# Optimization experiments

Measured on AMD Instinct MI355X. Metric: run time of the kernel, lower is better.

Reference implementation:

```python
import jax, jax.numpy as jnp
import numpy as np
import math

B, L, H, NH = 8, 512, 512, 8
DH = H // NH


def setup_inputs() -> dict:
    key = jax.random.key(0)
    ks = jax.random.split(key, 12)
    src = jax.random.normal(ks[0], (B, L, H), dtype=jnp.float32)
    seq_len = jax.random.randint(ks[1], (B,), L // 2, L + 1).astype(jnp.int32)
    seq_len = seq_len.at[0].set(L)  # guarantee max(seq_len) == L
    pe = jax.random.normal(ks[2], (2 * L, H), dtype=jnp.float32) * 0.02
    s = 1.0 / math.sqrt(H)
    Wq = jax.random.normal(ks[3], (H, H), dtype=jnp.float32) * s
    bq = jnp.zeros((H,), jnp.float32)
    Wk = jax.random.normal(ks[4], (H, H), dtype=jnp.float32) * s
    bk = jnp.zeros((H,), jnp.float32)
    Wv = jax.random.normal(ks[5], (H, H), dtype=jnp.float32) * s
    bv = jnp.zeros((H,), jnp.float32)
    Wr = jax.random.normal(ks[6], (H, H), dtype=jnp.float32) * s
    br = jnp.zeros((H,), jnp.float32)
    u = jax.random.normal(ks[7], (NH, DH), dtype=jnp.float32) * 0.02
    v = jax.random.normal(ks[8], (NH, DH), dtype=jnp.float32) * 0.02
    gamma = jnp.ones((H,), jnp.float32)
    beta = jnp.zeros((H,), jnp.float32)
    return dict(src=src, seq_len=seq_len, pe=pe, Wq=Wq, bq=bq, Wk=Wk, bk=bk,
                Wv=Wv, bv=bv, Wr=Wr, br=br, u=u, v=v, gamma=gamma, beta=beta)


def reference(src, seq_len, pe, Wq, bq, Wk, bk, Wv, bv, Wr, br, u, v, gamma, beta):
    b, l, h = src.shape
    dh = h // NH
    # relative distance rel[i,j] = j - i, lookup pe[rel + L]  -> [L, L, H]
    rel = jnp.arange(l)[None, :] - jnp.arange(l)[:, None]
    R = pe[rel + l]
    # projections (torch Linear: y = x W^T + b)
    q = src @ Wq.T + bq
    k = src @ Wk.T + bk
    val = src @ Wv.T + bv
    R = R @ Wr.T + br
    # split heads
    q = q.reshape(b, l, NH, dh)
    k = k.reshape(b, l, NH, dh)
    val = val.reshape(b, l, NH, dh)
    R = R.reshape(l, l, NH, dh)
    # Transformer-XL score terms
    A = jnp.einsum('bihd,bjhd->bhij', q, k)
    Bt = jnp.einsum('bihd,ijhd->bhij', q, R)
    C = jnp.einsum('hd,bjhd->bhj', u, k)[:, :, None, :]
    D = jnp.einsum('ijhd,hd->hij', R, v)[None]
    scores = (A + Bt + C + D) / math.sqrt(dh)
    # key-side padding mask
    mask = jnp.arange(l)[None, :] < seq_len[:, None]  # [B, L]
    scores = jnp.where(mask[:, None, None, :], scores, jnp.float32(-1e15))
    attn = jax.nn.softmax(scores, axis=-1)
    out = jnp.einsum('bhij,bjhd->bihd', attn, val).reshape(b, l, h)
    res = src + out
    # LayerNorm (eps=1e-5) then exact GELU
    mu = jnp.mean(res, axis=-1, keepdims=True)
    var = jnp.mean((res - mu) ** 2, axis=-1, keepdims=True)
    ln = (res - mu) * jax.lax.rsqrt(var + 1e-5) * gamma + beta
    return jax.nn.gelu(ln, approximate=False)
```

## Files before the change

### kernel.cpp

```cpp
#include <hip/hip_runtime.h>
#include <math.h>

#define Bn 8
#define Ln 512
#define Hn 512
#define NHn 8
#define DHn 64

typedef __attribute__((ext_vector_type(8))) short short8;
typedef __attribute__((ext_vector_type(4))) float f32x4;

__device__ __forceinline__ unsigned short f2bf(float f) {
    unsigned int u = __float_as_uint(f);
    unsigned int r = (u + 0x7FFFu + ((u >> 16) & 1u)) >> 16;
    return (unsigned short)r;
}
__device__ __forceinline__ float bf2f(unsigned short s) {
    return __uint_as_float(((unsigned int)s) << 16);
}

__device__ __forceinline__ void gload_lds16(const void* g, void* l) {
    __builtin_amdgcn_global_load_lds(
        (const __attribute__((address_space(1))) unsigned int*)g,
        (__attribute__((address_space(3))) unsigned int*)l,
        16, 0, 0);
}

__global__ __launch_bounds__(256) void convert_kernel(
    const float* __restrict__ src, const float* __restrict__ pe,
    const float* __restrict__ Wq, const float* __restrict__ Wk,
    const float* __restrict__ Wv, const float* __restrict__ Wr,
    const float* __restrict__ bq, const float* __restrict__ bk,
    const float* __restrict__ bv,
    unsigned short* __restrict__ src_bf, unsigned short* __restrict__ pe_bf,
    unsigned short* __restrict__ Wcat_bf, unsigned short* __restrict__ Wr_bf,
    float* __restrict__ bcat)
{
    const int bid = blockIdx.x;
    const int tid = threadIdx.x;
    const float* in; unsigned short* outp; int base4;
    if (bid < 2048)      { in = src; outp = src_bf;           base4 = bid; }
    else if (bid < 2560) { in = pe;  outp = pe_bf;            base4 = bid - 2048; }
    else if (bid < 2816) { in = Wq;  outp = Wcat_bf;          base4 = bid - 2560; }
    else if (bid < 3072) { in = Wk;  outp = Wcat_bf + 262144; base4 = bid - 2816; }
    else if (bid < 3328) { in = Wv;  outp = Wcat_bf + 524288; base4 = bid - 3072; }
    else if (bid < 3584) { in = Wr;  outp = Wr_bf;            base4 = bid - 3328; }
    else {
        const int idx = (bid - 3584) * 256 + tid;
        if (idx < 512)            bcat[idx] = bq[idx];
        else if (idx < 1024)      bcat[idx] = bk[idx - 512];
        else if (idx < 1536)      bcat[idx] = bv[idx - 1024];
        return;
    }
    const int i4 = (base4 * 256 + tid) * 4;
    float4 x = *(const float4*)&in[i4];
    ushort4 o;
    o.x = f2bf(x.x); o.y = f2bf(x.y); o.z = f2bf(x.z); o.w = f2bf(x.w);
    *(ushort4*)&outp[i4] = o;
}

__global__ __launch_bounds__(256) void mfma_nt_kernel(
    const unsigned short* __restrict__ A0, const unsigned short* __restrict__ B0,
    const float* __restrict__ bias0, unsigned short* __restrict__ C0, int ldc0,
    const unsigned short* __restrict__ A1, const unsigned short* __restrict__ B1,
    const float* __restrict__ bias1, unsigned short* __restrict__ C1, int ldc1)
{
    const unsigned short* A; const unsigned short* B; const float* bias;
    unsigned short* C; int ldc;
    if (blockIdx.z == 0) {
        A = A0; B = B0; bias = bias0; C = C0; ldc = ldc0;
    } else {
        if (blockIdx.x >= 4 || blockIdx.y >= 8) return;
        A = A1; B = B1; bias = bias1; C = C1; ldc = ldc1;
    }

    __shared__ unsigned short As[128 * 32];
    __shared__ unsigned short Bs[128 * 32];

    const int m0 = blockIdx.y * 128;
    const int n0 = blockIdx.x * 128;
    const int t = threadIdx.x;
    const int wave = t >> 6, lane = t & 63;
    const int wm = (wave >> 1) * 64;
    const int wn = (wave & 1) * 64;

    f32x4 acc[4][4] = {};

    const int srow = wave * 32 + (lane >> 2);
    const int scol = (lane & 3) * 8;
    const unsigned short* Ag = A + (size_t)(m0 + srow) * 512 + scol;
    const unsigned short* Bg = B + (size_t)(n0 + srow) * 512 + scol;
    unsigned short* AsW = &As[srow * 32 + scol];
    unsigned short* BsW = &Bs[srow * 32 + scol];

    for (int k0 = 0; k0 < 512; k0 += 32) {
        __syncthreads();
        gload_lds16(Ag + k0,            AsW);
        gload_lds16(Ag + k0 + 16 * 512, AsW + 16 * 32);
        gload_lds16(Bg + k0,            BsW);
        gload_lds16(Bg + k0 + 16 * 512, BsW + 16 * 32);
        __syncthreads();

        short8 af[4], bf[4];
        #pragma unroll
        for (int mt = 0; mt < 4; ++mt)
            af[mt] = *(const short8*)&As[(wm + mt * 16 + (lane & 15)) * 32 + (lane >> 4) * 8];
        #pragma unroll
        for (int nt = 0; nt < 4; ++nt)
            bf[nt] = *(const short8*)&Bs[(wn + nt * 16 + (lane & 15)) * 32 + (lane >> 4) * 8];
        #pragma unroll
        for (int mt = 0; mt < 4; ++mt)
            #pragma unroll
            for (int nt = 0; nt < 4; ++nt)
                acc[mt][nt] = __builtin_amdgcn_mfma_f32_16x16x32_bf16(
                    af[mt], bf[nt], acc[mt][nt], 0, 0, 0);
    }

    const int crow = (lane >> 4) * 4;
    const int ccol = lane & 15;
    #pragma unroll
    for (int mt = 0; mt < 4; ++mt)
        #pragma unroll
        for (int nt = 0; nt < 4; ++nt) {
            const int n = n0 + wn + nt * 16 + ccol;
            const float bn = bias[n];
            #pragma unroll
            for (int r = 0; r < 4; ++r) {
                const int m = m0 + wm + mt * 16 + crow + r;
                C[(size_t)m * ldc + n] = f2bf(acc[mt][nt][r] + bn);
            }
        }
}

#define PADK 72
__global__ __launch_bounds__(256) void attn_kernel(
    const unsigned short* __restrict__ QKVb,
    const unsigned short* __restrict__ Rpb,
    const float* __restrict__ u, const float* __restrict__ v,
    const int* __restrict__ seq_len, float* __restrict__ O)
{
    const int i0 = blockIdx.x * 64;
    const int h  = blockIdx.y;
    const int b  = blockIdx.z;
    const int slen = seq_len[b];

    __shared__ unsigned short k_s [64 * PADK];
    __shared__ unsigned short vT_s[64 * PADK];
    __shared__ unsigned short rs_s[128 * PADK];
    __shared__ unsigned short p_s [4 * 16 * PADK];
    __shared__ unsigned short qrT [4 * 128 * 20];

    const int t = threadIdx.x;
    const int wave = t >> 6, lane = t & 63;
    const int l = lane & 15, g = lane >> 4;

    short8 af_qu[2], af_qv[2];
    {
        const unsigned short* qrow =
            QKVb + (size_t)(b * 512 + i0 + wave * 16 + l) * 1536 + h * 64;
        #pragma unroll
        for (int kk = 0; kk < 2; ++kk) {
            const int c = kk * 32 + g * 8;
            unsigned short q8[8];
            *(uint4*)q8 = *(const uint4*)(qrow + c);
            float4 u0 = *(const float4*)(u + h * 64 + c);
            float4 u1 = *(const float4*)(u + h * 64 + c + 4);
            float4 v0 = *(const float4*)(v + h * 64 + c);
            float4 v1 = *(const float4*)(v + h * 64 + c + 4);
            float uf[8] = {u0.x,u0.y,u0.z,u0.w,u1.x,u1.y,u1.z,u1.w};
            float vf[8] = {v0.x,v0.y,v0.z,v0.w,v1.x,v1.y,v1.z,v1.w};
            short8 qu, qv;
            #pragma unroll
            for (int e = 0; e < 8; ++e) {
                float qf = bf2f(q8[e]);
                qu[e] = (short)f2bf(qf + uf[e]);
                qv[e] = (short)f2bf(qf + vf[e]);
            }
            af_qu[kk] = qu; af_qv[kk] = qv;
        }
    }

    float m_run[4], l_run[4];
    f32x4 accO[4] = {};
    #pragma unroll
    for (int r = 0; r < 4; ++r) { m_run[r] = -3.0e38f; l_run[r] = 0.f; }

    const int dmin = i0 ? (0 - i0 + 449) : 449;

    for (int j0 = 0; j0 < 512; j0 += 64) {
        __syncthreads();

        {
            const int jr = t >> 2, c0 = (t & 3) * 16;
            const unsigned short* base =
                QKVb + (size_t)(b * 512 + j0 + jr) * 1536 + h * 64;
            uint4 kv0 = *(const uint4*)(base + 512 + c0);
            uint4 kv1 = *(const uint4*)(base + 512 + c0 + 8);
            *(uint4*)(k_s + jr * PADK + c0)     = kv0;
            *(uint4*)(k_s + jr * PADK + c0 + 8) = kv1;
            unsigned short vt[16];
            *(uint4*)vt       = *(const uint4*)(base + 1024 + c0);
            *(uint4*)(vt + 8) = *(const uint4*)(base + 1024 + c0 + 8);
            #pragma unroll
            for (int m = 0; m < 16; ++m)
                vT_s[(c0 + m) * PADK + jr] = vt[m];
        }
        {
            const int r = t >> 1, c0 = (t & 1) * 32;
            int grow = j0 - i0 + 449 + r;
            if (grow > 1023) grow = 1023;
            const unsigned short* rp = Rpb + (size_t)grow * 512 + h * 64 + c0;
            #pragma unroll
            for (int e = 0; e < 4; ++e)
                *(uint4*)(rs_s + r * PADK + c0 + e * 8) = *(const uint4*)(rp + e * 8);
        }
        __syncthreads();

        f32x4 accA[4];
        #pragma unroll
        for (int nt = 0; nt < 4; ++nt) {
            f32x4 a = {};
            #pragma unroll
            for (int kk = 0; kk < 2; ++kk) {
                short8 bk = *(const short8*)&k_s[(nt * 16 + l) * PADK + kk * 32 + g * 8];
                a = __builtin_amdgcn_mfma_f32_16x16x32_bf16(af_qu[kk], bk, a, 0, 0, 0);
            }
            accA[nt] = a;
        }

        #pragma unroll
        for (int nt8 = 0; nt8 < 8; ++nt8) {
            f32x4 a = {};
            #pragma unroll
            for (int kk = 0; kk < 2; ++kk) {
                short8 br8 = *(const short8*)&rs_s[(nt8 * 16 + l) * PADK + kk * 32 + g * 8];
                a = __builtin_amdgcn_mfma_f32_16x16x32_bf16(af_qv[kk], br8, a, 0, 0, 0);
            }
            ushort4 w4;
            w4.x = f2bf(a[0]); w4.y = f2bf(a[1]); w4.z = f2bf(a[2]); w4.w = f2bf(a[3]);
            *(ushort4*)(qrT + ((size_t)wave * 128 + nt8 * 16 + l) * 20 + g * 4) = w4;
        }
        __builtin_amdgcn_sched_barrier(0);

        float sv[4][4];
        #pragma unroll
        for (int nt = 0; nt < 4; ++nt)
            #pragma unroll
            for (int r = 0; r < 4; ++r) {
                const int i16 = g * 4 + r;
                const int band = nt * 16 + l - (wave * 16 + i16) + 63;
                const float qr = bf2f(qrT[((size_t)wave * 128 + band) * 20 + i16]);
                float s = (accA[nt][r] + qr) * 0.125f;
                if (j0 + nt * 16 + l >= slen) s = -1e15f;
                sv[nt][r] = s;
            }

        float alpha_r[4];
        #pragma unroll
        for (int r = 0; r < 4; ++r) {
            float tm = fmaxf(fmaxf(sv[0][r], sv[1][r]), fmaxf(sv[2][r], sv[3][r]));
            tm = fmaxf(tm, __shfl_xor(tm, 1, 64));
            tm = fmaxf(tm, __shfl_xor(tm, 2, 64));
            tm = fmaxf(tm, __shfl_xor(tm, 4, 64));
            tm = fmaxf(tm, __shfl_xor(tm, 8, 64));
            const float mn = fmaxf(m_run[r], tm);
            alpha_r[r] = __expf(m_run[r] - mn);
            m_run[r] = mn;
            float ss = 0.f;
            #pragma unroll
            for (int nt = 0; nt < 4; ++nt) {
                const float p = __expf(sv[nt][r] - mn);
                sv[nt][r] = p; ss += p;
            }
            ss += __shfl_xor(ss, 1, 64);
            ss += __shfl_xor(ss, 2, 64);
            ss += __shfl_xor(ss, 4, 64);
            ss += __shfl_xor(ss, 8, 64);
            l_run[r] = l_run[r] * alpha_r[r] + ss;
        }

        #pragma unroll
        for (int nt = 0; nt < 4; ++nt)
            #pragma unroll
            for (int r = 0; r < 4; ++r)
                p_s[((size_t)wave * 16 + g * 4 + r) * PADK + nt * 16 + l] = f2bf(sv[nt][r]);
        __builtin_amdgcn_sched_barrier(0);

        #pragma unroll
        for (int nt = 0; nt < 4; ++nt)
            #pragma unroll
            for (int r = 0; r < 4; ++r)
                accO[nt][r] *= alpha_r[r];

        short8 pa[2];
        #pragma unroll
        for (int kk = 0; kk < 2; ++kk)
            pa[kk] = *(const short8*)&p_s[((size_t)wave * 16 + l) * PADK + kk * 32 + g * 8];
        #pragma unroll
        for (int nt = 0; nt < 4; ++nt) {
            #pragma unroll
            for (int kk = 0; kk < 2; ++kk) {
                short8 bv8 = *(const short8*)&vT_s[(nt * 16 + l) * PADK + kk * 32 + g * 8];
                accO[nt] = __builtin_amdgcn_mfma_f32_16x16x32_bf16(pa[kk], bv8, accO[nt], 0, 0, 0);
            }
        }
    }

    float inv[4];
    #pragma unroll
    for (int r = 0; r < 4; ++r) inv[r] = 1.0f / l_run[r];
    #pragma unroll
    for (int nt = 0; nt < 4; ++nt)
        #pragma unroll
        for (int r = 0; r < 4; ++r)
            O[(size_t)(b * 512 + i0 + wave * 16 + g * 4 + r) * 512 + h * 64 + nt * 16 + l]
                = accO[nt][r] * inv[r];
}

__global__ __launch_bounds__(256) void ln_gelu_kernel(
    const float* __restrict__ src, const float* __restrict__ O,
    const float* __restrict__ gamma, const float* __restrict__ beta,
    float* __restrict__ out)
{
    const int row  = blockIdx.x * 4 + (threadIdx.x >> 6);
    const int lane = threadIdx.x & 63;
    const float* s = &src[(size_t)row * 512];
    const float* o = &O[(size_t)row * 512];
    float x[8];
    float sum = 0.f;
    #pragma unroll
    for (int e = 0; e < 8; ++e) {
        x[e] = s[lane + e * 64] + o[lane + e * 64];
        sum += x[e];
    }
    #pragma unroll
    for (int off = 32; off >= 1; off >>= 1) sum += __shfl_xor(sum, off, 64);
    const float mean = sum * (1.0f / 512.0f);
    float var = 0.f;
    #pragma unroll
    for (int e = 0; e < 8; ++e) { float d = x[e] - mean; var += d * d; }
    #pragma unroll
    for (int off = 32; off >= 1; off >>= 1) var += __shfl_xor(var, off, 64);
    var *= (1.0f / 512.0f);
    const float inv = rsqrtf(var + 1e-5f);
    #pragma unroll
    for (int e = 0; e < 8; ++e) {
        const int c = lane + e * 64;
        float ln = (x[e] - mean) * inv * gamma[c] + beta[c];
        out[(size_t)row * 512 + c] = 0.5f * ln * (1.0f + erff(ln * 0.70710678118654752f));
    }
}

extern "C" void kernel_launch(void* const* d_in, const int* in_sizes, int n_in,
                              void* d_out, int out_size, void* d_ws, size_t ws_size,
                              hipStream_t stream)
{
    const float* src     = (const float*)d_in[0];
    const int*   seq_len = (const int*)  d_in[1];
    const float* pe      = (const float*)d_in[2];
    const float* Wq      = (const float*)d_in[3];
    const float* bq      = (const float*)d_in[4];
    const float* Wk      = (const float*)d_in[5];
    const float* bk      = (const float*)d_in[6];
    const float* Wv      = (const float*)d_in[7];
    const float* bv      = (const float*)d_in[8];
    const float* Wr      = (const float*)d_in[9];
    const float* br      = (const float*)d_in[10];
    const float* u       = (const float*)d_in[11];
    const float* v       = (const float*)d_in[12];
    const float* gamma   = (const float*)d_in[13];
    const float* beta    = (const float*)d_in[14];
    float* out = (float*)d_out;

    char* w = (char*)d_ws;
    unsigned short* QKVb    = (unsigned short*)(w);
    unsigned short* Rpb     = (unsigned short*)(w + 12582912);
    float*          O       = (float*)         (w + 13631488);
    unsigned short* src_bf  = (unsigned short*)(w + 22020096);
    unsigned short* pe_bf   = (unsigned short*)(w + 26214400);
    unsigned short* Wcat_bf = (unsigned short*)(w + 27262976);
    unsigned short* Wr_bf   = (unsigned short*)(w + 28835840);
    float*          bcat    = (float*)         (w + 29360128);

    convert_kernel<<<dim3(3590), 256, 0, stream>>>(
        src, pe, Wq, Wk, Wv, Wr, bq, bk, bv,
        src_bf, pe_bf, Wcat_bf, Wr_bf, bcat);

    mfma_nt_kernel<<<dim3(12, 32, 2), 256, 0, stream>>>(
        src_bf, Wcat_bf, bcat, QKVb, 1536,
        pe_bf,  Wr_bf,   br,   Rpb,  512);

    attn_kernel<<<dim3(8, NHn, Bn), 256, 0, stream>>>(QKVb, Rpb, u, v, seq_len, O);

    ln_gelu_kernel<<<dim3(Bn * Ln / 4), 256, 0, stream>>>(src, O, gamma, beta, out);
}
```

Baseline: 145.7 us.

## Emit transposed V from projection GEMM and use rolling ring buffer for relative-position scores

The projection GEMM now writes Q/K into a narrower buffer and writes V already transposed into a separate global layout. This lets the attention kernel load V tiles with vector copies instead of scattered per-element LDS transposes. The attention kernel also replaces the per-tile 128-row R window with a 128-slot ring buffer of q·R products, computing only 64 new relative rows per tile (128 on the first). That roughly halves the R-side MFMA work and LDS traffic, at the cost of extra barriers and a more complex slot indexing scheme.

New measurement: 142.1 us. -2.5%, faster.

```diff
diff --git a/kernel.cpp b/kernel.cpp
--- a/kernel.cpp
+++ b/kernel.cpp
@@ -60,25 +60,35 @@
 }
 
 __global__ __launch_bounds__(256) void mfma_nt_kernel(
-    const unsigned short* __restrict__ A0, const unsigned short* __restrict__ B0,
-    const float* __restrict__ bias0, unsigned short* __restrict__ C0, int ldc0,
-    const unsigned short* __restrict__ A1, const unsigned short* __restrict__ B1,
-    const float* __restrict__ bias1, unsigned short* __restrict__ C1, int ldc1)
+    const unsigned short* __restrict__ src_bf,
+    const unsigned short* __restrict__ Wcat_bf,
+    const float* __restrict__ bcat,
+    unsigned short* __restrict__ QKb,
+    unsigned short* __restrict__ VTg,
+    const unsigned short* __restrict__ pe_bf,
+    const unsigned short* __restrict__ Wr_bf,
+    const float* __restrict__ br,
+    unsigned short* __restrict__ Rpb)
 {
-    const unsigned short* A; const unsigned short* B; const float* bias;
-    unsigned short* C; int ldc;
+    const unsigned short* A; const unsigned short* B;
+    int m0, n0, mode;
     if (blockIdx.z == 0) {
-        A = A0; B = B0; bias = bias0; C = C0; ldc = ldc0;
+        if (blockIdx.x < 8) {
+            mode = 0; A = src_bf;  m0 = blockIdx.y * 128;
+            B = Wcat_bf; n0 = blockIdx.x * 128;
+        } else {
+            mode = 1; A = Wcat_bf; m0 = blockIdx.x * 128;
+            B = src_bf;  n0 = blockIdx.y * 128;
+        }
     } else {
         if (blockIdx.x >= 4 || blockIdx.y >= 8) return;
-        A = A1; B = B1; bias = bias1; C = C1; ldc = ldc1;
+        mode = 2; A = pe_bf; m0 = blockIdx.y * 128;
+        B = Wr_bf; n0 = blockIdx.x * 128;
     }
 
     __shared__ unsigned short As[128 * 32];
     __shared__ unsigned short Bs[128 * 32];
 
-    const int m0 = blockIdx.y * 128;
-    const int n0 = blockIdx.x * 128;
     const int t = threadIdx.x;
     const int wave = t >> 6, lane = t & 63;
     const int wm = (wave >> 1) * 64;
@@ -118,23 +128,52 @@
 
     const int crow = (lane >> 4) * 4;
     const int ccol = lane & 15;
-    #pragma unroll
-    for (int mt = 0; mt < 4; ++mt)
-        #pragma unroll
-        for (int nt = 0; nt < 4; ++nt) {
-            const int n = n0 + wn + nt * 16 + ccol;
-            const float bn = bias[n];
-            #pragma unroll
-            for (int r = 0; r < 4; ++r) {
-                const int m = m0 + wm + mt * 16 + crow + r;
-                C[(size_t)m * ldc + n] = f2bf(acc[mt][nt][r] + bn);
-            }
-        }
+    if (mode == 0) {
+        #pragma unroll
+        for (int mt = 0; mt < 4; ++mt)
+            #pragma unroll
+            for (int nt = 0; nt < 4; ++nt) {
+                const int n = n0 + wn + nt * 16 + ccol;
+                const float bn = bcat[n];
+                #pragma unroll
+                for (int r = 0; r < 4; ++r) {
+                    const int m = m0 + wm + mt * 16 + crow + r;
+                    QKb[(size_t)m * 1024 + n] = f2bf(acc[mt][nt][r] + bn);
+                }
+            }
+    } else if (mode == 1) {
+        #pragma unroll
+        for (int mt = 0; mt < 4; ++mt)
+            #pragma unroll
+            for (int nt = 0; nt < 4; ++nt) {
+                const int n = n0 + wn + nt * 16 + ccol;
+                #pragma unroll
+                for (int r = 0; r < 4; ++r) {
+                    const int m = m0 + wm + mt * 16 + crow + r;
+                    VTg[(size_t)(m - 1024) * 4096 + n] = f2bf(acc[mt][nt][r] + bcat[m]);
+                }
+            }
+    } else {
+        #pragma unroll
+        for (int mt = 0; mt < 4; ++mt)
+            #pragma unroll
+            for (int nt = 0; nt < 4; ++nt) {
+                const int n = n0 + wn + nt * 16 + ccol;
+                const float bn = br[n];
+                #pragma unroll
+                for (int r = 0; r < 4; ++r) {
+                    const int m = m0 + wm + mt * 16 + crow + r;
+                    Rpb[(size_t)m * 512 + n] = f2bf(acc[mt][nt][r] + bn);
+                }
+            }
+    }
 }
 
 #define PADK 72
+#define QRS 133
 __global__ __launch_bounds__(256) void attn_kernel(
-    const unsigned short* __restrict__ QKVb,
+    const unsigned short* __restrict__ QKb,
+    const unsigned short* __restrict__ VTg,
     const unsigned short* __restrict__ Rpb,
     const float* __restrict__ u, const float* __restrict__ v,
     const int* __restrict__ seq_len, float* __restrict__ O)
@@ -146,9 +185,9 @@
 
     __shared__ unsigned short k_s [64 * PADK];
     __shared__ unsigned short vT_s[64 * PADK];
-    __shared__ unsigned short rs_s[128 * PADK];
-    __shared__ unsigned short p_s [4 * 16 * PADK];
-    __shared__ unsigned short qrT [4 * 128 * 20];
+    __shared__ unsigned short rs_s[64 * PADK];
+    __shared__ unsigned short p_s [64 * PADK];
+    __shared__ unsigned short qrT [64 * QRS];
 
     const int t = threadIdx.x;
     const int wave = t >> 6, lane = t & 63;
@@ -157,7 +196,7 @@
     short8 af_qu[2], af_qv[2];
     {
         const unsigned short* qrow =
-            QKVb + (size_t)(b * 512 + i0 + wave * 16 + l) * 1536 + h * 64;
+            QKb + (size_t)(b * 512 + i0 + wave * 16 + l) * 1024 + h * 64;
         #pragma unroll
         for (int kk = 0; kk < 2; ++kk) {
             const int c = kk * 32 + g * 8;
@@ -185,34 +224,48 @@
     #pragma unroll
     for (int r = 0; r < 4; ++r) { m_run[r] = -3.0e38f; l_run[r] = 0.f; }
 
-    const int dmin = i0 ? (0 - i0 + 449) : 449;
-
-    for (int j0 = 0; j0 < 512; j0 += 64) {
+    const int jr = t >> 2, c0 = (t & 3) * 16;
+
+    for (int jt = 0; jt < 8; ++jt) {
+        const int j0 = jt * 64;
         __syncthreads();
 
         {
-            const int jr = t >> 2, c0 = (t & 3) * 16;
-            const unsigned short* base =
-                QKVb + (size_t)(b * 512 + j0 + jr) * 1536 + h * 64;
-            uint4 kv0 = *(const uint4*)(base + 512 + c0);
-            uint4 kv1 = *(const uint4*)(base + 512 + c0 + 8);
-            *(uint4*)(k_s + jr * PADK + c0)     = kv0;
-            *(uint4*)(k_s + jr * PADK + c0 + 8) = kv1;
-            unsigned short vt[16];
-            *(uint4*)vt       = *(const uint4*)(base + 1024 + c0);
-            *(uint4*)(vt + 8) = *(const uint4*)(base + 1024 + c0 + 8);
-            #pragma unroll
-            for (int m = 0; m < 16; ++m)
-                vT_s[(c0 + m) * PADK + jr] = vt[m];
-        }
-        {
-            const int r = t >> 1, c0 = (t & 1) * 32;
-            int grow = j0 - i0 + 449 + r;
-            if (grow > 1023) grow = 1023;
-            const unsigned short* rp = Rpb + (size_t)grow * 512 + h * 64 + c0;
-            #pragma unroll
-            for (int e = 0; e < 4; ++e)
-                *(uint4*)(rs_s + r * PADK + c0 + e * 8) = *(const uint4*)(rp + e * 8);
+            const unsigned short* kp =
+                QKb + (size_t)(b * 512 + j0 + jr) * 1024 + 512 + h * 64 + c0;
+            *(uint4*)(k_s + jr * PADK + c0)     = *(const uint4*)(kp);
+            *(uint4*)(k_s + jr * PADK + c0 + 8) = *(const uint4*)(kp + 8);
+            const unsigned short* vp =
+                VTg + (size_t)(h * 64 + jr) * 4096 + b * 512 + j0 + c0;
+            *(uint4*)(vT_s + jr * PADK + c0)     = *(const uint4*)(vp);
+            *(uint4*)(vT_s + jr * PADK + c0 + 8) = *(const uint4*)(vp + 8);
+        }
+
+        const int nchunk = (jt == 0) ? 2 : 1;
+        for (int c = 0; c < nchunk; ++c) {
+            const int g_base = (jt == 0) ? (448 - i0 + 64 * c) : (j0 - i0 + 512);
+            {
+                const unsigned short* rp =
+                    Rpb + (size_t)(g_base + jr) * 512 + h * 64 + c0;
+                *(uint4*)(rs_s + jr * PADK + c0)     = *(const uint4*)(rp);
+                *(uint4*)(rs_s + jr * PADK + c0 + 8) = *(const uint4*)(rp + 8);
+            }
+            __syncthreads();
+            const int slot0 = (g_base & 127);
+            #pragma unroll
+            for (int nt8 = 0; nt8 < 4; ++nt8) {
+                f32x4 a = {};
+                #pragma unroll
+                for (int kk = 0; kk < 2; ++kk) {
+                    short8 br8 = *(const short8*)&rs_s[(nt8 * 16 + l) * PADK + kk * 32 + g * 8];
+                    a = __builtin_amdgcn_mfma_f32_16x16x32_bf16(af_qv[kk], br8, a, 0, 0, 0);
+                }
+                const int sl = slot0 + nt8 * 16 + l;
+                #pragma unroll
+                for (int r = 0; r < 4; ++r)
+                    qrT[(wave * 16 + g * 4 + r) * QRS + sl] = f2bf(a[r]);
+            }
+            if (c + 1 < nchunk) __syncthreads();
         }
         __syncthreads();
 
@@ -228,28 +281,14 @@
             accA[nt] = a;
         }
 
-        #pragma unroll
-        for (int nt8 = 0; nt8 < 8; ++nt8) {
-            f32x4 a = {};
-            #pragma unroll
-            for (int kk = 0; kk < 2; ++kk) {
-                short8 br8 = *(const short8*)&rs_s[(nt8 * 16 + l) * PADK + kk * 32 + g * 8];
-                a = __builtin_amdgcn_mfma_f32_16x16x32_bf16(af_qv[kk], br8, a, 0, 0, 0);
-            }
-            ushort4 w4;
-            w4.x = f2bf(a[0]); w4.y = f2bf(a[1]); w4.z = f2bf(a[2]); w4.w = f2bf(a[3]);
-            *(ushort4*)(qrT + ((size_t)wave * 128 + nt8 * 16 + l) * 20 + g * 4) = w4;
-        }
-        __builtin_amdgcn_sched_barrier(0);
-
         float sv[4][4];
         #pragma unroll
         for (int nt = 0; nt < 4; ++nt)
             #pragma unroll
             for (int r = 0; r < 4; ++r) {
-                const int i16 = g * 4 + r;
-                const int band = nt * 16 + l - (wave * 16 + i16) + 63;
-                const float qr = bf2f(qrT[((size_t)wave * 128 + band) * 20 + i16]);
+                const int il = wave * 16 + g * 4 + r;
+                const int slot = (j0 + nt * 16 + l - i0 - il + 512) & 127;
+                const float qr = bf2f(qrT[il * QRS + slot]);
                 float s = (accA[nt][r] + qr) * 0.125f;
                 if (j0 + nt * 16 + l >= slen) s = -1e15f;
                 sv[nt][r] = s;
@@ -283,7 +322,7 @@
         for (int nt = 0; nt < 4; ++nt)
             #pragma unroll
             for (int r = 0; r < 4; ++r)
-                p_s[((size_t)wave * 16 + g * 4 + r) * PADK + nt * 16 + l] = f2bf(sv[nt][r]);
+                p_s[(wave * 16 + g * 4 + r) * PADK + nt * 16 + l] = f2bf(sv[nt][r]);
         __builtin_amdgcn_sched_barrier(0);
 
         #pragma unroll
@@ -295,7 +334,7 @@
         short8 pa[2];
         #pragma unroll
         for (int kk = 0; kk < 2; ++kk)
-            pa[kk] = *(const short8*)&p_s[((size_t)wave * 16 + l) * PADK + kk * 32 + g * 8];
+            pa[kk] = *(const short8*)&p_s[(wave * 16 + l) * PADK + kk * 32 + g * 8];
         #pragma unroll
         for (int nt = 0; nt < 4; ++nt) {
             #pragma unroll
@@ -373,7 +412,8 @@
     float* out = (float*)d_out;
 
     char* w = (char*)d_ws;
-    unsigned short* QKVb    = (unsigned short*)(w);
+    unsigned short* QKb     = (unsigned short*)(w);
+    unsigned short* VTg     = (unsigned short*)(w + 8388608);
     unsigned short* Rpb     = (unsigned short*)(w + 12582912);
     float*          O       = (float*)         (w + 13631488);
     unsigned short* src_bf  = (unsigned short*)(w + 22020096);
@@ -387,10 +427,10 @@
         src_bf, pe_bf, Wcat_bf, Wr_bf, bcat);
 
     mfma_nt_kernel<<<dim3(12, 32, 2), 256, 0, stream>>>(
-        src_bf, Wcat_bf, bcat, QKVb, 1536,
-        pe_bf,  Wr_bf,   br,   Rpb,  512);
-
-    attn_kernel<<<dim3(8, NHn, Bn), 256, 0, stream>>>(QKVb, Rpb, u, v, seq_len, O);
+        src_bf, Wcat_bf, bcat, QKb, VTg,
+        pe_bf, Wr_bf, br, Rpb);
+
+    attn_kernel<<<dim3(8, NHn, Bn), 256, 0, stream>>>(QKb, VTg, Rpb, u, v, seq_len, O);
 
     ln_gelu_kernel<<<dim3(Bn * Ln / 4), 256, 0, stream>>>(src, O, gamma, beta, out);
 }
```
